# Performance work log

Measured on AMD Instinct MI355X. Metric: run time of the kernel, lower is better.

The kernel has to match this reference:

```python
import jax, jax.numpy as jnp
import numpy as np

WS = (2, 6, 12)          # window (Wz, Wh, Ww)
SHIFT = (1, 3, 6)        # Wz//2, Wh//2, Ww//2
NUM_HEADS = 8
DIM = 256
HIDDEN = 1024            # mlp_ratio * dim
TYPE_OF_WINDOWS = 64     # (Z//Wz)*(H//Wh)
EPS = 1e-5


def _build_position_index(ws):
    Wz, Wh, Ww = ws
    zi = np.arange(Wz); zj = -np.arange(Wz) * Wz
    hi = np.arange(Wh); hj = -np.arange(Wh) * Wh
    w = np.arange(Ww)
    gzi, ghi, gw = np.meshgrid(zi, hi, w, indexing='ij')
    gzj, ghj, _ = np.meshgrid(zj, hj, w, indexing='ij')
    fi = np.stack([gzi.ravel(), ghi.ravel(), gw.ravel()])
    fj = np.stack([gzj.ravel(), ghj.ravel(), gw.ravel()])
    coords = fi[:, :, None] - fj[:, None, :]
    coords[2] += Ww - 1
    coords[1] *= 2 * Ww - 1
    coords[0] *= (2 * Ww - 1) * Wh * Wh
    return coords.sum(0).reshape(-1)  # (N*N,) int


def _window_partition(x, ws):
    # (B, Z, H, W, C) -> (B*n_windows, Wz*Wh*Ww, C)
    B, Z, H, W, C = x.shape
    Wz, Wh, Ww = ws
    x = x.reshape(B, Z // Wz, Wz, H // Wh, Wh, W // Ww, Ww, C)
    x = x.transpose(0, 1, 3, 5, 2, 4, 6, 7)
    return x.reshape(-1, Wz * Wh * Ww, C)


def _window_reverse(win, ws, B, Z, H, W):
    Wz, Wh, Ww = ws
    x = win.reshape(B, Z // Wz, H // Wh, W // Ww, Wz, Wh, Ww, -1)
    x = x.transpose(0, 1, 4, 2, 5, 3, 6, 7)
    return x.reshape(B, Z, H, W, -1)


def _build_shift_mask(Z, H, W, ws, shift):
    Wz, Wh, Ww = ws
    sz, sh, sw = shift
    img = np.zeros((1, Z, H, W, 1), dtype=np.float32)
    z_slices = (slice(0, -Wz), slice(-Wz, -sz), slice(-sz, None))
    h_slices = (slice(0, -Wh), slice(-Wh, -sh), slice(-sh, None))
    w_slices = (slice(0, -Ww), slice(-Ww, -sw), slice(-sw, None))
    cnt = 0
    for zs in z_slices:
        for hs in h_slices:
            for wsl in w_slices:
                img[:, zs, hs, wsl, :] = cnt
                cnt += 1
    m = _window_partition(img, ws)[..., 0]             # (n_w, N)
    am = m[:, None, :] - m[:, :, None]                 # (n_w, N, N)
    am = np.where(am != 0, -100.0, 0.0).astype(np.float32)
    return am[:, None]                                 # (n_w, 1, N, N)


def _ln(x, g, b):
    mu = x.mean(-1, keepdims=True)
    var = ((x - mu) ** 2).mean(-1, keepdims=True)
    return (x - mu) * jax.lax.rsqrt(var + EPS) * g + b


def setup_inputs() -> dict:
    key = jax.random.key(0)
    ks = jax.random.split(key, 16)
    B, Z, H, W, C = 1, 8, 96, 192, DIM
    n_unique = (2 * WS[2] - 1) * WS[1] * WS[1] * WS[0] * WS[0]  # 3312
    s = 0.02
    return {
        'x': jax.random.normal(ks[0], (B, Z * H * W, C), jnp.float32),
        'g1': jnp.ones((C,), jnp.float32),
        'beta1': jnp.zeros((C,), jnp.float32),
        'wqkv': jax.random.normal(ks[1], (3 * C, C), jnp.float32) * s,
        'bqkv': jnp.zeros((3 * C,), jnp.float32),
        'bias_table': jax.random.normal(ks[2], (n_unique, TYPE_OF_WINDOWS, NUM_HEADS), jnp.float32) * s,
        'wproj': jax.random.normal(ks[3], (C, C), jnp.float32) * s,
        'bproj': jnp.zeros((C,), jnp.float32),
        'g2': jnp.ones((C,), jnp.float32),
        'beta2': jnp.zeros((C,), jnp.float32),
        'w1': jax.random.normal(ks[4], (HIDDEN, C), jnp.float32) * s,
        'b1': jnp.zeros((HIDDEN,), jnp.float32),
        'w2': jax.random.normal(ks[5], (C, HIDDEN), jnp.float32) * s,
        'b2': jnp.zeros((C,), jnp.float32),
        'Z': Z, 'H': H, 'W': W, 'window_type_index': 0,
    }


def reference(x, g1, beta1, wqkv, bqkv, bias_table, wproj, bproj, g2, beta2,
              w1, b1, w2, b2, Z, H, W, window_type_index):
    B, L, C = x.shape
    hd = C // NUM_HEADS
    scale = hd ** (-0.5)
    N = WS[0] * WS[1] * WS[2]

    xs = _ln(x, g1, beta1).reshape(B, Z, H, W, C)
    # shift
    xs = jnp.roll(xs, (-SHIFT[0], -SHIFT[1], -SHIFT[2]), axis=(1, 2, 3))
    mask = jnp.asarray(_build_shift_mask(Z, H, W, WS, SHIFT))  # (n_w,1,N,N)

    win = _window_partition(xs, WS)                    # (Bw, N, C)
    Bw = win.shape[0]
    qkv = (win @ wqkv.T + bqkv).reshape(Bw, N, 3, NUM_HEADS, hd).transpose(2, 0, 3, 1, 4)
    q, k, v = qkv[0], qkv[1], qkv[2]                   # (Bw, h, N, hd)

    attn = jnp.einsum('bhnd,bhmd->bhnm', q * scale, k)
    pos_index = _build_position_index(WS)              # (N*N,)
    bias = bias_table[pos_index, window_type_index]    # (N*N, heads)
    bias = bias.reshape(N, N, NUM_HEADS).transpose(2, 0, 1)[None]
    attn = attn + bias

    n_w = mask.shape[0]
    attn = attn.reshape(B, n_w, NUM_HEADS, N, N) + mask[None]
    attn = jax.nn.softmax(attn, axis=-1).reshape(Bw, NUM_HEADS, N, N)

    out = jnp.einsum('bhnm,bhmd->bhnd', attn, v).transpose(0, 2, 1, 3).reshape(Bw, N, C)
    out = out @ wproj.T + bproj

    xr = _window_reverse(out, WS, B, Z, H, W)
    xr = jnp.roll(xr, SHIFT, axis=(1, 2, 3)).reshape(B, Z * H * W, C)

    x = x + xr
    h = _ln(x, g2, beta2)
    h = jax.nn.gelu(h @ w1.T + b1, approximate=False)
    h = h @ w2.T + b2
    return x + h
```

## Files before the change

kernel.cpp:

```cpp
#include <hip/hip_runtime.h>
#include <hip/hip_bf16.h>
#include <math.h>

#define L_TOK   147456
#define CDIM    256
#define C3      768
#define HID     1024
#define NWIN    1024
#define NTOK    144
#define NHEADS  8
#define HD      32
#define SCALE   0.1767766952966369f

typedef __attribute__((ext_vector_type(8))) short bfrag;
typedef __attribute__((ext_vector_type(4))) float f32x4;

__device__ __forceinline__ ushort f2bf(float f) {
    __hip_bfloat16 h = __float2bfloat16(f);
    return *reinterpret_cast<ushort*>(&h);
}
__device__ __forceinline__ float bf2f(ushort u) {
    __hip_bfloat16 h = *reinterpret_cast<__hip_bfloat16*>(&u);
    return __bfloat162float(h);
}

__device__ __forceinline__ void gld16(const ushort* g, ushort* l) {
    __builtin_amdgcn_global_load_lds(
        (const __attribute__((address_space(1))) void*)g,
        (__attribute__((address_space(3))) void*)l, 16, 0, 0);
}

__device__ __forceinline__ int shift_src(int gt) {
    const int win = gt / NTOK;
    const int nt  = gt - win * NTOK;
    const int wz = win >> 8, wh = (win >> 4) & 15, ww = win & 15;
    const int lz = nt / 72;
    const int t2 = nt - lz * 72;
    const int lh = t2 / 12, lw = t2 - lh * 12;
    const int z = (wz * 2 + lz + 1) & 7;
    int h = wh * 6 + lh + 3;  if (h >= 96)  h -= 96;
    int w = ww * 12 + lw + 6; if (w >= 192) w -= 192;
    return (z * 96 + h) * 192 + w;
}

__global__ __launch_bounds__(256) void ln1_kernel(const float* __restrict__ x,
                                                  const float* __restrict__ g,
                                                  const float* __restrict__ b,
                                                  ushort* __restrict__ xw,
                                                  int row0)
{
    const int wave = threadIdx.x >> 6;
    const int lane = threadIdx.x & 63;
    const int t = blockIdx.x * 4 + wave;
    const int src = shift_src(row0 + t);
    const float4 xv = *(const float4*)(x + (size_t)src * CDIM + lane * 4);
    float s  = xv.x + xv.y + xv.z + xv.w;
    float ss = xv.x*xv.x + xv.y*xv.y + xv.z*xv.z + xv.w*xv.w;
    #pragma unroll
    for (int off = 32; off; off >>= 1) {
        s  += __shfl_xor(s,  off);
        ss += __shfl_xor(ss, off);
    }
    const float mean = s * (1.0f / CDIM);
    const float var  = ss * (1.0f / CDIM) - mean * mean;
    const float rstd = rsqrtf(var + 1e-5f);
    const float4 gv = *(const float4*)(g + lane * 4);
    const float4 bv = *(const float4*)(b + lane * 4);
    union { ushort u[4]; uint2 q; } pk;
    pk.u[0] = f2bf((xv.x - mean) * rstd * gv.x + bv.x);
    pk.u[1] = f2bf((xv.y - mean) * rstd * gv.y + bv.y);
    pk.u[2] = f2bf((xv.z - mean) * rstd * gv.z + bv.z);
    pk.u[3] = f2bf((xv.w - mean) * rstd * gv.w + bv.w);
    *(uint2*)(xw + (size_t)t * CDIM + lane * 4) = pk.q;
}

__global__ __launch_bounds__(256) void cvt_kernel(const float* __restrict__ s,
                                                  ushort* __restrict__ d)
{
    const int i = (blockIdx.x * 256 + threadIdx.x) * 4;
    const float4 v = *(const float4*)(s + i);
    d[i + 0] = f2bf(v.x); d[i + 1] = f2bf(v.y);
    d[i + 2] = f2bf(v.z); d[i + 3] = f2bf(v.w);
}

__global__ __launch_bounds__(256) void comb_pre_kernel(const float* __restrict__ bt,
                                                       const int* __restrict__ wti_p,
                                                       ushort* __restrict__ comb)
{
    const int e = blockIdx.x * 256 + threadIdx.x;
    const int wti = *wti_p;
    const int reg  = e & 3;
    const int lane = (e >> 2) & 63;
    const int t    = e >> 8;
    const int ct = t % 9;
    const int rb = (t / 9) % 9;
    const int h  = (t / 81) % 8;
    const int cls = t / 648;
    const int i = rb * 16 + ((lane >> 4) << 2) + reg;
    const int j = ct * 16 + (lane & 15);
    const int zi = i / 72, ri = i - zi * 72, hi = ri / 12, wi = ri - (ri / 12) * 12;
    const int zj = j / 72, rj = j - zj * 72, hj = rj / 12, wj = rj - (rj / 12) * 12;
    const int idx = (zi + 2 * zj) * 828 + (hi + 6 * hj) * 23 + (wi - wj + 11);
    const float bias = bt[((size_t)idx * 64 + wti) * 8 + h];
    const int cz = (cls >> 2) & 1, ch = (cls >> 1) & 1, cw = cls & 1;
    const int ri_ = (cz ? (zi == 0 ? 1 : 2) : 0) * 9
                  + (ch ? (hi < 3 ? 1 : 2) : 0) * 3
                  + (cw ? (wi < 6 ? 1 : 2) : 0);
    const int rj_ = (cz ? (zj == 0 ? 1 : 2) : 0) * 9
                  + (ch ? (hj < 3 ? 1 : 2) : 0) * 3
                  + (cw ? (wj < 6 ? 1 : 2) : 0);
    comb[e] = f2bf(bias + ((ri_ == rj_) ? 0.0f : -100.0f));
}

__global__ __launch_bounds__(64) void attn_kernel(const ushort* __restrict__ qkv,
                                                  const ushort* __restrict__ comb,
                                                  ushort* __restrict__ outb,
                                                  int win0)
{
    __shared__ ushort vt[32][168];
    __shared__ ushort pt[16][168];

    const int winl = blockIdx.x >> 3;
    const int head = blockIdx.x & 7;
    const int win  = win0 + winl;
    const int lane = threadIdx.x;
    const int g = lane >> 4, c = lane & 15;
    const int cls = (((win >> 8) == 3) ? 4 : 0)
                  | ((((win >> 4) & 15) == 15) ? 2 : 0)
                  | (((win & 15) == 15) ? 1 : 0);

    const ushort* qb = qkv + (((size_t)(winl * 3 + 0) * 8 + head) * NTOK) * HD;
    const ushort* kb = qkv + (((size_t)(winl * 3 + 1) * 8 + head) * NTOK) * HD;
    const ushort* vb = qkv + (((size_t)(winl * 3 + 2) * 8 + head) * NTOK) * HD;

    for (int i = lane; i < 512; i += 64) vt[i >> 4][144 + (i & 15)] = 0;
    for (int i = lane; i < 256; i += 64) pt[i >> 4][144 + (i & 15)] = 0;
    for (int base = lane * 8; base < NTOK * HD; base += 512) {
        const int j = base >> 5, d0 = base & 31;
        union { ushort u[8]; uint4 q; } tv;
        tv.q = *(const uint4*)(vb + base);
        #pragma unroll
        for (int e = 0; e < 8; ++e) vt[d0 + e][j] = tv.u[e];
    }
    __syncthreads();

    bfrag kf[9];
    #pragma unroll
    for (int ct = 0; ct < 9; ++ct)
        kf[ct] = *(const bfrag*)(kb + (size_t)(ct * 16 + c) * HD + g * 8);
    bfrag vf[2][5];
    #pragma unroll
    for (int nt = 0; nt < 2; ++nt)
        #pragma unroll
        for (int kt = 0; kt < 5; ++kt)
            vf[nt][kt] = *(const bfrag*)&vt[nt * 16 + c][kt * 32 + g * 8];

    const ushort* cb = comb + ((size_t)cls * 8 + head) * 81 * 256;

    for (int rb = 0; rb < 9; ++rb) {
        const bfrag aq = *(const bfrag*)(qb + (size_t)(rb * 16 + c) * HD + g * 8);
        f32x4 s[9];
        #pragma unroll
        for (int ct = 0; ct < 9; ++ct)
            s[ct] = __builtin_amdgcn_mfma_f32_16x16x32_bf16(
                aq, kf[ct], (f32x4){0.0f, 0.0f, 0.0f, 0.0f}, 0, 0, 0);

        #pragma unroll
        for (int ct = 0; ct < 9; ++ct) {
            const uint2 bw = *(const uint2*)(cb + (size_t)(rb * 9 + ct) * 256 + lane * 4);
            s[ct][0] += bf2f((ushort)(bw.x & 0xffff));
            s[ct][1] += bf2f((ushort)(bw.x >> 16));
            s[ct][2] += bf2f((ushort)(bw.y & 0xffff));
            s[ct][3] += bf2f((ushort)(bw.y >> 16));
        }

        float mx[4] = {-1e30f, -1e30f, -1e30f, -1e30f};
        #pragma unroll
        for (int ct = 0; ct < 9; ++ct)
            #pragma unroll
            for (int r = 0; r < 4; ++r) mx[r] = fmaxf(mx[r], s[ct][r]);
        #pragma unroll
        for (int off = 1; off < 16; off <<= 1)
            #pragma unroll
            for (int r = 0; r < 4; ++r) mx[r] = fmaxf(mx[r], __shfl_xor(mx[r], off));
        float sm[4] = {0.0f, 0.0f, 0.0f, 0.0f};
        #pragma unroll
        for (int ct = 0; ct < 9; ++ct)
            #pragma unroll
            for (int r = 0; r < 4; ++r) {
                const float e = __expf(s[ct][r] - mx[r]);
                s[ct][r] = e; sm[r] += e;
            }
        #pragma unroll
        for (int off = 1; off < 16; off <<= 1)
            #pragma unroll
            for (int r = 0; r < 4; ++r) sm[r] += __shfl_xor(sm[r], off);
        float inv[4];
        #pragma unroll
        for (int r = 0; r < 4; ++r) inv[r] = 1.0f / sm[r];

        #pragma unroll
        for (int ct = 0; ct < 9; ++ct)
            #pragma unroll
            for (int r = 0; r < 4; ++r)
                pt[g * 4 + r][ct * 16 + c] = f2bf(s[ct][r]);

        f32x4 o[2] = {(f32x4){0,0,0,0}, (f32x4){0,0,0,0}};
        #pragma unroll
        for (int kt = 0; kt < 5; ++kt) {
            const bfrag pa = *(const bfrag*)&pt[c][kt * 32 + g * 8];
            o[0] = __builtin_amdgcn_mfma_f32_16x16x32_bf16(pa, vf[0][kt], o[0], 0, 0, 0);
            o[1] = __builtin_amdgcn_mfma_f32_16x16x32_bf16(pa, vf[1][kt], o[1], 0, 0, 0);
        }

        const size_t ob = ((size_t)winl * NTOK + rb * 16 + g * 4) * CDIM + head * HD;
        #pragma unroll
        for (int nt = 0; nt < 2; ++nt)
            #pragma unroll
            for (int r = 0; r < 4; ++r)
                outb[ob + (size_t)r * CDIM + nt * 16 + c] = f2bf(o[nt][r] * inv[r]);
    }
}

template<int EPI>
__global__ __launch_bounds__(256) void mgemm(const ushort* __restrict__ A,
                                             const ushort* __restrict__ Bw,
                                             const float* __restrict__ bias,
                                             void* __restrict__ outp,
                                             const float* __restrict__ resid,
                                             int K, int grow0)
{
    __shared__ __align__(16) ushort Asb[128 * 64];
    __shared__ __align__(16) ushort Bsb[128 * 64];

    const int tid = threadIdx.x;
    const int m0 = blockIdx.x * 128;
    const int n0 = blockIdx.y * 128;
    const int w = tid >> 6, lane = tid & 63;
    const int wm = w >> 1, wn = w & 1;
    const int fr = lane & 15, kg = lane >> 4;
    const int wbase = tid & 192;

    f32x4 acc[4][4];
    #pragma unroll
    for (int i = 0; i < 4; ++i)
        #pragma unroll
        for (int j = 0; j < 4; ++j)
            acc[i][j] = (f32x4){0.0f, 0.0f, 0.0f, 0.0f};

    int lrow[4], lsl[4];
    #pragma unroll
    for (int it = 0; it < 4; ++it) {
        const int s = it * 256 + tid;
        lrow[it] = s >> 3;
        lsl[it]  = ((s & 7) ^ (lrow[it] & 7)) * 8;
    }

    size_t aoff[4], boff[4];
    #pragma unroll
    for (int it = 0; it < 4; ++it) {
        aoff[it] = (size_t)(m0 + lrow[it]) * K;
        boff[it] = (size_t)(n0 + lrow[it]) * K;
    }

    for (int kt = 0; kt < K; kt += 64) {
        #pragma unroll
        for (int it = 0; it < 4; ++it)
            gld16(A + aoff[it] + kt + lsl[it], &Asb[(it * 256 + wbase) * 8]);
        #pragma unroll
        for (int it = 0; it < 4; ++it)
            gld16(Bw + boff[it] + kt + lsl[it], &Bsb[(it * 256 + wbase) * 8]);
        __syncthreads();

        #pragma unroll
        for (int kh = 0; kh < 2; ++kh) {
            bfrag af[4], bfv[4];
            #pragma unroll
            for (int fm = 0; fm < 4; ++fm) {
                const int r = wm * 64 + fm * 16 + fr;
                af[fm] = *(const bfrag*)&Asb[r * 64 + (((kh * 4 + kg) ^ (r & 7)) * 8)];
            }
            #pragma unroll
            for (int fn = 0; fn < 4; ++fn) {
                const int r = wn * 64 + fn * 16 + fr;
                bfv[fn] = *(const bfrag*)&Bsb[r * 64 + (((kh * 4 + kg) ^ (r & 7)) * 8)];
            }
            #pragma unroll
            for (int fm = 0; fm < 4; ++fm)
                #pragma unroll
                for (int fn = 0; fn < 4; ++fn)
                    acc[fm][fn] = __builtin_amdgcn_mfma_f32_16x16x32_bf16(
                        af[fm], bfv[fn], acc[fm][fn], 0, 0, 0);
        }
        __syncthreads();
    }

    #pragma unroll
    for (int fn = 0; fn < 4; ++fn) {
        const int col = n0 + wn * 64 + fn * 16 + fr;
        const float bv = bias[col];
        #pragma unroll
        for (int fm = 0; fm < 4; ++fm) {
            #pragma unroll
            for (int r = 0; r < 4; ++r) {
                const int mi = m0 + wm * 64 + fm * 16 + kg * 4 + r;
                float val = acc[fm][fn][r] + bv;
                if constexpr (EPI == 0) {
                    if (col < 256) val *= SCALE;
                    const int winl = mi / NTOK, nt = mi - (mi / NTOK) * NTOK;
                    const int sel = col >> 8, head = (col >> 5) & 7, d = col & 31;
                    ((ushort*)outp)[(((size_t)(winl * 3 + sel) * 8 + head) * NTOK + nt) * HD + d] = f2bf(val);
                } else {
                    const int p = shift_src(grow0 + mi);
                    ((float*)outp)[(size_t)p * CDIM + col] = resid[(size_t)p * CDIM + col] + val;
                }
            }
        }
    }
}

__global__ __launch_bounds__(512) void mlp_fused(float* __restrict__ io,
                                                 const ushort* __restrict__ w1b,
                                                 const float* __restrict__ b1,
                                                 const ushort* __restrict__ w2b,
                                                 const float* __restrict__ b2,
                                                 const float* __restrict__ g2,
                                                 const float* __restrict__ beta2)
{
    __shared__ __align__(16) ushort lds[40960];
    ushort* XS = lds;
    ushort* HS = lds + 16384;
    ushort* SB = lds + 24576;

    const int tid = threadIdx.x;
    const int w = tid >> 6, lane = tid & 63;
    const int wm = w >> 2, wn = w & 3;
    const int fr = lane & 15, kg = lane >> 4;
    const int wbase = tid & 0x1C0;
    const int grow0 = blockIdx.x * 64;

    {
        const int row = tid >> 3;
        const int oct = tid & 7;
        const float* xr = io + (size_t)(grow0 + row) * CDIM + oct * 32;
        float4 v[8];
        float s = 0.0f, ss = 0.0f;
        #pragma unroll
        for (int j = 0; j < 8; ++j) {
            v[j] = *(const float4*)(xr + j * 4);
            s  += v[j].x + v[j].y + v[j].z + v[j].w;
            ss += v[j].x*v[j].x + v[j].y*v[j].y + v[j].z*v[j].z + v[j].w*v[j].w;
        }
        #pragma unroll
        for (int off = 1; off < 8; off <<= 1) {
            s  += __shfl_xor(s,  off);
            ss += __shfl_xor(ss, off);
        }
        const float mean = s * (1.0f / CDIM);
        const float var  = ss * (1.0f / CDIM) - mean * mean;
        const float rstd = rsqrtf(var + 1e-5f);
        #pragma unroll
        for (int j = 0; j < 4; ++j) {
            const int c = oct * 32 + j * 8;
            const float4 ga = *(const float4*)(g2 + c);
            const float4 gb = *(const float4*)(g2 + c + 4);
            const float4 ba = *(const float4*)(beta2 + c);
            const float4 bb = *(const float4*)(beta2 + c + 4);
            union { ushort u[8]; uint4 q4; } pk;
            pk.u[0] = f2bf((v[2*j].x   - mean) * rstd * ga.x + ba.x);
            pk.u[1] = f2bf((v[2*j].y   - mean) * rstd * ga.y + ba.y);
            pk.u[2] = f2bf((v[2*j].z   - mean) * rstd * ga.z + ba.z);
            pk.u[3] = f2bf((v[2*j].w   - mean) * rstd * ga.w + ba.w);
            pk.u[4] = f2bf((v[2*j+1].x - mean) * rstd * gb.x + bb.x);
            pk.u[5] = f2bf((v[2*j+1].y - mean) * rstd * gb.y + bb.y);
            pk.u[6] = f2bf((v[2*j+1].z - mean) * rstd * gb.z + bb.z);
            pk.u[7] = f2bf((v[2*j+1].w - mean) * rstd * gb.w + bb.w);
            const int slot = oct * 4 + j;
            *(uint4*)&XS[row * 256 + (slot ^ (row & 7)) * 8] = pk.q4;
        }
    }

    f32x4 acc[2][4];
    #pragma unroll
    for (int i = 0; i < 2; ++i)
        #pragma unroll
        for (int j = 0; j < 4; ++j)
            acc[i][j] = (f32x4){0.0f, 0.0f, 0.0f, 0.0f};

    for (int s = 0; s < 8; ++s) {
        f32x4 c1[2][2];
        #pragma unroll
        for (int i = 0; i < 2; ++i) { c1[i][0] = (f32x4){0,0,0,0}; c1[i][1] = (f32x4){0,0,0,0}; }
        for (int kt = 0; kt < 4; ++kt) {
            __syncthreads();
            #pragma unroll
            for (int i = 0; i < 2; ++i) {
                const int slot = i * 512 + tid;
                const int row = slot >> 3;
                const int sl = (slot & 7) ^ (row & 7);
                gld16(w1b + (size_t)(s * 128 + row) * 256 + kt * 64 + sl * 8,
                      &SB[(i * 512 + wbase) * 8]);
            }
            __syncthreads();
            #pragma unroll
            for (int ks = 0; ks < 2; ++ks) {
                bfrag af[2], bf2[2];
                #pragma unroll
                for (int fm = 0; fm < 2; ++fm) {
                    const int r = wm * 32 + fm * 16 + fr;
                    const int slot = kt * 8 + ks * 4 + kg;
                    af[fm] = *(const bfrag*)&XS[r * 256 + (slot ^ (r & 7)) * 8];
                }
                #pragma unroll
                for (int fn = 0; fn < 2; ++fn) {
                    const int r = wn * 32 + fn * 16 + fr;
                    const int slot = ks * 4 + kg;
                    bf2[fn] = *(const bfrag*)&SB[r * 64 + (slot ^ (r & 7)) * 8];
                }
                #pragma unroll
                for (int fm = 0; fm < 2; ++fm)
                    #pragma unroll
                    for (int fn = 0; fn < 2; ++fn)
                        c1[fm][fn] = __builtin_amdgcn_mfma_f32_16x16x32_bf16(
                            af[fm], bf2[fn], c1[fm][fn], 0, 0, 0);
            }
        }
        #pragma unroll
        for (int fn = 0; fn < 2; ++fn) {
            const int colh = wn * 32 + fn * 16 + fr;
            const float b1v = b1[s * 128 + colh];
            #pragma unroll
            for (int fm = 0; fm < 2; ++fm) {
                #pragma unroll
                for (int r = 0; r < 4; ++r) {
                    const int mi = wm * 32 + fm * 16 + kg * 4 + r;
                    const float v = c1[fm][fn][r] + b1v;
                    const float ge = 0.5f * v * (1.0f + erff(v * 0.70710678118654752f));
                    const int hv = f2bf(ge);
                    const int ov = __shfl_xor(hv, 1);
                    if ((fr & 1) == 0) {
                        const int idx = mi * 128 + ((colh >> 3) ^ (mi & 7)) * 8 + (colh & 7);
                        *(uint*)&HS[idx] = (uint)(hv & 0xffff) | ((uint)(ov & 0xffff) << 16);
                    }
                }
            }
        }
        for (int kt2 = 0; kt2 < 2; ++kt2) {
            __syncthreads();
            #pragma unroll
            for (int i = 0; i < 4; ++i) {
                const int slot = i * 512 + tid;
                const int row = slot >> 3;
                const int sl = (slot & 7) ^ (row & 7);
                gld16(w2b + (size_t)row * 1024 + s * 128 + kt2 * 64 + sl * 8,
                      &SB[(i * 512 + wbase) * 8]);
            }
            __syncthreads();
            #pragma unroll
            for (int ks = 0; ks < 2; ++ks) {
                bfrag af[2], bf4[4];
                #pragma unroll
                for (int fm = 0; fm < 2; ++fm) {
                    const int r = wm * 32 + fm * 16 + fr;
                    const int slot = kt2 * 8 + ks * 4 + kg;
                    af[fm] = *(const bfrag*)&HS[r * 128 + (slot ^ (r & 7)) * 8];
                }
                #pragma unroll
                for (int fn = 0; fn < 4; ++fn) {
                    const int r = wn * 64 + fn * 16 + fr;
                    const int slot = ks * 4 + kg;
                    bf4[fn] = *(const bfrag*)&SB[r * 64 + (slot ^ (r & 7)) * 8];
                }
                #pragma unroll
                for (int fm = 0; fm < 2; ++fm)
                    #pragma unroll
                    for (int fn = 0; fn < 4; ++fn)
                        acc[fm][fn] = __builtin_amdgcn_mfma_f32_16x16x32_bf16(
                            af[fm], bf4[fn], acc[fm][fn], 0, 0, 0);
            }
        }
    }

    #pragma unroll
    for (int fn = 0; fn < 4; ++fn) {
        const int col = wn * 64 + fn * 16 + fr;
        const float bv = b2[col];
        #pragma unroll
        for (int fm = 0; fm < 2; ++fm) {
            #pragma unroll
            for (int r = 0; r < 4; ++r) {
                const int mi = wm * 32 + fm * 16 + kg * 4 + r;
                const size_t gi = (size_t)(grow0 + mi) * CDIM + col;
                io[gi] += acc[fm][fn][r] + bv;
            }
        }
    }
}

extern "C" void kernel_launch(void* const* d_in, const int* in_sizes, int n_in,
                              void* d_out, int out_size, void* d_ws, size_t ws_size,
                              hipStream_t stream)
{
    const float* x     = (const float*)d_in[0];
    const float* g1    = (const float*)d_in[1];
    const float* beta1 = (const float*)d_in[2];
    const float* wqkv  = (const float*)d_in[3];
    const float* bqkv  = (const float*)d_in[4];
    const float* btab  = (const float*)d_in[5];
    const float* wproj = (const float*)d_in[6];
    const float* bproj = (const float*)d_in[7];
    const float* g2    = (const float*)d_in[8];
    const float* beta2 = (const float*)d_in[9];
    const float* w1    = (const float*)d_in[10];
    const float* b1    = (const float*)d_in[11];
    const float* w2    = (const float*)d_in[12];
    const float* b2    = (const float*)d_in[13];
    const int*   wti   = (const int*)d_in[17];
    float* out = (float*)d_out;

    const size_t COMB_ELEMS = (size_t)8 * 8 * 81 * 256;
    const size_t WQKV_E = (size_t)C3 * CDIM, WP_E = (size_t)CDIM * CDIM;
    const size_t W1_E = (size_t)HID * CDIM,  W2_E = (size_t)CDIM * HID;
    const size_t base_bytes = COMB_ELEMS * 2
                            + (WQKV_E + WP_E + W1_E + W2_E) * 2;

    int nch = 32;
    for (int cand : {4, 8, 16, 32}) {
        const size_t rows = (size_t)L_TOK / cand;
        if (base_bytes + rows * (C3 + CDIM) * 2 <= ws_size) { nch = cand; break; }
    }
    const int wins_per = NWIN / nch;
    const int rows_per = wins_per * NTOK;

    char* wsp = (char*)d_ws;
    ushort* comb = (ushort*)wsp; wsp += COMB_ELEMS * 2;
    ushort* wq_b = (ushort*)wsp; wsp += WQKV_E * 2;
    ushort* wp_b = (ushort*)wsp; wsp += WP_E * 2;
    ushort* w1_b = (ushort*)wsp; wsp += W1_E * 2;
    ushort* w2_b = (ushort*)wsp; wsp += W2_E * 2;
    ushort* ratt = (ushort*)wsp; wsp += (size_t)rows_per * CDIM * 2;
    ushort* rbig = (ushort*)wsp;

    cvt_kernel<<<(int)(WQKV_E / 1024), 256, 0, stream>>>(wqkv, wq_b);
    cvt_kernel<<<(int)(WP_E   / 1024), 256, 0, stream>>>(wproj, wp_b);
    cvt_kernel<<<(int)(W1_E   / 1024), 256, 0, stream>>>(w1, w1_b);
    cvt_kernel<<<(int)(W2_E   / 1024), 256, 0, stream>>>(w2, w2_b);
    comb_pre_kernel<<<(int)(COMB_ELEMS / 256), 256, 0, stream>>>(btab, wti, comb);

    for (int c = 0; c < nch; ++c) {
        const int row0 = c * rows_per;
        const int win0 = c * wins_per;
        ln1_kernel<<<rows_per / 4, 256, 0, stream>>>(x, g1, beta1, ratt, row0);
        mgemm<0><<<dim3(rows_per / 128, C3 / 128), 256, 0, stream>>>(
            ratt, wq_b, bqkv, rbig, nullptr, CDIM, row0);
        attn_kernel<<<wins_per * NHEADS, 64, 0, stream>>>(rbig, comb, ratt, win0);
        mgemm<1><<<dim3(rows_per / 128, CDIM / 128), 256, 0, stream>>>(
            ratt, wp_b, bproj, out, x, CDIM, row0);
    }

    mlp_fused<<<L_TOK / 64, 512, 0, stream>>>(out, w1_b, b1, w2_b, b2, g2, beta2);
}
```

Measured before the change: 766.5 us.

## Shrink fused MLP tile to 32 rows with 256 threads and swap GEMM grid order

The fused MLP kernel now processes 32 tokens per block with 4 waves instead of 64 tokens with 8 waves. This halves LDS use to allow more resident blocks, and the second GEMM now loads weight tiles in 32-wide K slices with a new swizzle. Separately, the mgemm grid is transposed so consecutive blocks share the same A row tile across output columns, which should improve cache reuse. The trade-off is that each weight tile is now reused by fewer rows, so total weight traffic per token doubles.

Measured after the change: 799.0 us. +4.2%, slower.

```diff
diff --git a/kernel.cpp b/kernel.cpp
--- a/kernel.cpp
+++ b/kernel.cpp
@@ -234,8 +234,8 @@
     __shared__ __align__(16) ushort Bsb[128 * 64];
 
     const int tid = threadIdx.x;
-    const int m0 = blockIdx.x * 128;
-    const int n0 = blockIdx.y * 128;
+    const int m0 = blockIdx.y * 128;
+    const int n0 = blockIdx.x * 128;
     const int w = tid >> 6, lane = tid & 63;
     const int wm = w >> 1, wn = w & 1;
     const int fr = lane & 15, kg = lane >> 4;
@@ -319,7 +319,7 @@
     }
 }
 
-__global__ __launch_bounds__(512) void mlp_fused(float* __restrict__ io,
+__global__ __launch_bounds__(256) void mlp_fused(float* __restrict__ io,
                                                  const ushort* __restrict__ w1b,
                                                  const float* __restrict__ b1,
                                                  const ushort* __restrict__ w2b,
@@ -327,17 +327,16 @@
                                                  const float* __restrict__ g2,
                                                  const float* __restrict__ beta2)
 {
-    __shared__ __align__(16) ushort lds[40960];
+    __shared__ __align__(16) ushort lds[20480];
     ushort* XS = lds;
-    ushort* HS = lds + 16384;
-    ushort* SB = lds + 24576;
+    ushort* HS = lds + 8192;
+    ushort* SB = lds + 12288;
 
     const int tid = threadIdx.x;
-    const int w = tid >> 6, lane = tid & 63;
-    const int wm = w >> 2, wn = w & 3;
+    const int wn = tid >> 6, lane = tid & 63;
     const int fr = lane & 15, kg = lane >> 4;
-    const int wbase = tid & 0x1C0;
-    const int grow0 = blockIdx.x * 64;
+    const int wbase = tid & 192;
+    const int grow0 = blockIdx.x * 32;
 
     {
         const int row = tid >> 3;
@@ -394,20 +393,20 @@
         for (int kt = 0; kt < 4; ++kt) {
             __syncthreads();
             #pragma unroll
-            for (int i = 0; i < 2; ++i) {
-                const int slot = i * 512 + tid;
-                const int row = slot >> 3;
-                const int sl = (slot & 7) ^ (row & 7);
+            for (int i = 0; i < 4; ++i) {
+                const int L = i * 256 + tid;
+                const int row = L >> 3;
+                const int sl = (L & 7) ^ (row & 7);
                 gld16(w1b + (size_t)(s * 128 + row) * 256 + kt * 64 + sl * 8,
-                      &SB[(i * 512 + wbase) * 8]);
+                      &SB[(i * 256 + wbase) * 8]);
             }
             __syncthreads();
             #pragma unroll
             for (int ks = 0; ks < 2; ++ks) {
-                bfrag af[2], bf2[2];
+                bfrag af[2], bw[2];
                 #pragma unroll
                 for (int fm = 0; fm < 2; ++fm) {
-                    const int r = wm * 32 + fm * 16 + fr;
+                    const int r = fm * 16 + fr;
                     const int slot = kt * 8 + ks * 4 + kg;
                     af[fm] = *(const bfrag*)&XS[r * 256 + (slot ^ (r & 7)) * 8];
                 }
@@ -415,14 +414,14 @@
                 for (int fn = 0; fn < 2; ++fn) {
                     const int r = wn * 32 + fn * 16 + fr;
                     const int slot = ks * 4 + kg;
-                    bf2[fn] = *(const bfrag*)&SB[r * 64 + (slot ^ (r & 7)) * 8];
+                    bw[fn] = *(const bfrag*)&SB[r * 64 + (slot ^ (r & 7)) * 8];
                 }
                 #pragma unroll
                 for (int fm = 0; fm < 2; ++fm)
                     #pragma unroll
                     for (int fn = 0; fn < 2; ++fn)
                         c1[fm][fn] = __builtin_amdgcn_mfma_f32_16x16x32_bf16(
-                            af[fm], bf2[fn], c1[fm][fn], 0, 0, 0);
+                            af[fm], bw[fn], c1[fm][fn], 0, 0, 0);
             }
         }
         #pragma unroll
@@ -433,52 +432,43 @@
             for (int fm = 0; fm < 2; ++fm) {
                 #pragma unroll
                 for (int r = 0; r < 4; ++r) {
-                    const int mi = wm * 32 + fm * 16 + kg * 4 + r;
+                    const int mi = fm * 16 + kg * 4 + r;
                     const float v = c1[fm][fn][r] + b1v;
                     const float ge = 0.5f * v * (1.0f + erff(v * 0.70710678118654752f));
-                    const int hv = f2bf(ge);
-                    const int ov = __shfl_xor(hv, 1);
-                    if ((fr & 1) == 0) {
-                        const int idx = mi * 128 + ((colh >> 3) ^ (mi & 7)) * 8 + (colh & 7);
-                        *(uint*)&HS[idx] = (uint)(hv & 0xffff) | ((uint)(ov & 0xffff) << 16);
-                    }
+                    HS[mi * 128 + ((colh >> 3) ^ (mi & 7)) * 8 + (colh & 7)] = f2bf(ge);
                 }
             }
         }
-        for (int kt2 = 0; kt2 < 2; ++kt2) {
+        for (int kt2 = 0; kt2 < 4; ++kt2) {
             __syncthreads();
             #pragma unroll
             for (int i = 0; i < 4; ++i) {
-                const int slot = i * 512 + tid;
-                const int row = slot >> 3;
-                const int sl = (slot & 7) ^ (row & 7);
-                gld16(w2b + (size_t)row * 1024 + s * 128 + kt2 * 64 + sl * 8,
-                      &SB[(i * 512 + wbase) * 8]);
+                const int L = i * 256 + tid;
+                const int row = L >> 2;
+                const int sl = (L & 3) ^ ((row >> 1) & 3);
+                gld16(w2b + (size_t)row * 1024 + s * 128 + kt2 * 32 + sl * 8,
+                      &SB[(i * 256 + wbase) * 8]);
             }
             __syncthreads();
-            #pragma unroll
-            for (int ks = 0; ks < 2; ++ks) {
-                bfrag af[2], bf4[4];
+            bfrag af[2], bw[4];
+            #pragma unroll
+            for (int fm = 0; fm < 2; ++fm) {
+                const int r = fm * 16 + fr;
+                af[fm] = *(const bfrag*)&HS[r * 128 + (((kt2 * 4 + kg) ^ (r & 7)) * 8)];
+            }
+            #pragma unroll
+            for (int fn = 0; fn < 4; ++fn) {
+                const int r = wn * 64 + fn * 16 + fr;
+                bw[fn] = *(const bfrag*)&SB[r * 32 + ((kg ^ ((r >> 1) & 3)) * 8)];
+            }
+            #pragma unroll
+            for (int fm = 0; fm < 2; ++fm)
                 #pragma unroll
-                for (int fm = 0; fm < 2; ++fm) {
-                    const int r = wm * 32 + fm * 16 + fr;
-                    const int slot = kt2 * 8 + ks * 4 + kg;
-                    af[fm] = *(const bfrag*)&HS[r * 128 + (slot ^ (r & 7)) * 8];
-                }
-                #pragma unroll
-                for (int fn = 0; fn < 4; ++fn) {
-                    const int r = wn * 64 + fn * 16 + fr;
-                    const int slot = ks * 4 + kg;
-                    bf4[fn] = *(const bfrag*)&SB[r * 64 + (slot ^ (r & 7)) * 8];
-                }
-                #pragma unroll
-                for (int fm = 0; fm < 2; ++fm)
-                    #pragma unroll
-                    for (int fn = 0; fn < 4; ++fn)
-                        acc[fm][fn] = __builtin_amdgcn_mfma_f32_16x16x32_bf16(
-                            af[fm], bf4[fn], acc[fm][fn], 0, 0, 0);
-            }
-        }
+                for (int fn = 0; fn < 4; ++fn)
+                    acc[fm][fn] = __builtin_amdgcn_mfma_f32_16x16x32_bf16(
+                        af[fm], bw[fn], acc[fm][fn], 0, 0, 0);
+        }
+        __syncthreads();
     }
 
     #pragma unroll
@@ -489,7 +479,7 @@
         for (int fm = 0; fm < 2; ++fm) {
             #pragma unroll
             for (int r = 0; r < 4; ++r) {
-                const int mi = wm * 32 + fm * 16 + kg * 4 + r;
+                const int mi = fm * 16 + kg * 4 + r;
                 const size_t gi = (size_t)(grow0 + mi) * CDIM + col;
                 io[gi] += acc[fm][fn][r] + bv;
             }
@@ -551,12 +541,12 @@
         const int row0 = c * rows_per;
         const int win0 = c * wins_per;
         ln1_kernel<<<rows_per / 4, 256, 0, stream>>>(x, g1, beta1, ratt, row0);
-        mgemm<0><<<dim3(rows_per / 128, C3 / 128), 256, 0, stream>>>(
+        mgemm<0><<<dim3(C3 / 128, rows_per / 128), 256, 0, stream>>>(
             ratt, wq_b, bqkv, rbig, nullptr, CDIM, row0);
         attn_kernel<<<wins_per * NHEADS, 64, 0, stream>>>(rbig, comb, ratt, win0);
-        mgemm<1><<<dim3(rows_per / 128, CDIM / 128), 256, 0, stream>>>(
+        mgemm<1><<<dim3(CDIM / 128, rows_per / 128), 256, 0, stream>>>(
             ratt, wp_b, bproj, out, x, CDIM, row0);
     }
 
-    mlp_fused<<<L_TOK / 64, 512, 0, stream>>>(out, w1_b, b1, w2_b, b2, g2, beta2);
-}
+    mlp_fused<<<L_TOK / 32, 256, 0, stream>>>(out, w1_b, b1, w2_b, b2, g2, beta2);
+}
```
